# Performance work log

Measured on AMD Instinct MI355X. Metric: run time of the kernel, lower is better.

The kernel has to match this reference:

```python
import jax, jax.numpy as jnp
import numpy as np

N_NODES = 50000
N_EDGES = 400000
C = 32            # channels per irrep (scalars and l=1 vectors)
N_BASIS = 8
HID = 64          # radial MLP hidden dim
N_LAYERS = 2
N_SPECIES = 86
N_GRAPHS = 64
R_MAX = 5.0
EPS = 1e-5


def setup_inputs() -> dict:
    key = jax.random.key(0)
    ks = jax.random.split(key, 16)
    species = jax.random.randint(ks[0], (N_NODES,), 0, N_SPECIES)
    pos = jax.random.normal(ks[1], (N_NODES, 3), jnp.float32)
    edge_index = jax.random.randint(ks[2], (2, N_EDGES), 0, N_NODES)
    batch = jnp.sort(jax.random.randint(ks[3], (N_NODES,), 0, N_GRAPHS))

    emb = jax.random.normal(ks[4], (N_SPECIES, C), jnp.float32) * 0.1
    freqs = jnp.arange(1, N_BASIS + 1, dtype=jnp.float32) * jnp.pi / R_MAX  # trainable Bessel freqs
    rW1 = jax.random.normal(ks[5], (N_LAYERS, N_BASIS, HID), jnp.float32) / np.sqrt(N_BASIS)
    rb1 = jnp.zeros((N_LAYERS, HID), jnp.float32)
    rW2 = jax.random.normal(ks[6], (N_LAYERS, HID, HID), jnp.float32) / np.sqrt(HID)
    rb2 = jnp.zeros((N_LAYERS, HID), jnp.float32)
    rW3 = jax.random.normal(ks[7], (N_LAYERS, HID, 4 * C), jnp.float32) / np.sqrt(HID)
    rb3 = jnp.zeros((N_LAYERS, 4 * C), jnp.float32)
    Wss = jax.random.normal(ks[8], (N_LAYERS, C, C), jnp.float32) / np.sqrt(C)
    bss = jnp.zeros((N_LAYERS, C), jnp.float32)
    Wvv = jax.random.normal(ks[9], (N_LAYERS, C, C), jnp.float32) / np.sqrt(C)
    bn_gs = jnp.ones((N_LAYERS, C), jnp.float32)
    bn_bs = jnp.zeros((N_LAYERS, C), jnp.float32)
    bn_gv = jnp.ones((N_LAYERS, C), jnp.float32)
    W_out = jax.random.normal(ks[10], (C, 1), jnp.float32) / np.sqrt(C)
    b_out = jnp.zeros((1,), jnp.float32)
    atom_ref = jnp.zeros((N_SPECIES, 1), jnp.float32)  # AtomRef init zeros
    return dict(species=species, pos=pos, edge_index=edge_index, batch=batch,
                emb=emb, freqs=freqs, rW1=rW1, rb1=rb1, rW2=rW2, rb2=rb2,
                rW3=rW3, rb3=rb3, Wss=Wss, bss=bss, Wvv=Wvv,
                bn_gs=bn_gs, bn_bs=bn_bs, bn_gv=bn_gv,
                W_out=W_out, b_out=b_out, atom_ref=atom_ref)


def _bessel_basis(dist, freqs):
    # basis = sin(f*r)/r with smooth polynomial cutoff (as in BesselRadialBasis.forward)
    d = jnp.clip(dist, 0.0)
    basis = jnp.sin(freqs[None, :] * d[:, None]) / jnp.clip(d, 1e-6)[:, None]
    x = jnp.clip(d / R_MAX, 0.0, 1.0)
    cut = 1.0 - 6.0 * x ** 5 + 15.0 * x ** 4 - 10.0 * x ** 3
    cut = jnp.where(d <= R_MAX, cut, 0.0)
    return basis * cut[:, None]


def _forward(species, pos, edge_index, batch, emb, freqs, rW1, rb1, rW2, rb2,
             rW3, rb3, Wss, bss, Wvv, bn_gs, bn_bs, bn_gv, W_out, b_out, atom_ref):
    src, dst = edge_index[0], edge_index[1]
    vec = pos[dst] - pos[src]                      # (E,3) edge vectors
    dist = jnp.sqrt(jnp.sum(vec * vec, axis=-1))   # (E,)
    basis = _bessel_basis(dist, freqs)             # (E,NB)
    Y1 = vec / jnp.clip(dist, 1e-9)[:, None]       # (E,3) l=1 spherical harmonics (unit dir)

    s = emb[species]                               # (N,C) scalar features
    v = jnp.zeros((s.shape[0], C, 3), s.dtype)     # (N,C,3) l=1 features

    for l in range(N_LAYERS):
        # radial MLP -> per-edge channel-wise tensor-product weights (4 paths x C)
        h = jax.nn.silu(basis @ rW1[l] + rb1[l])
        h = jax.nn.silu(h @ rW2[l] + rb2[l])
        w = h @ rW3[l] + rb3[l]                    # (E,4C)
        w1, w2, w3, w4 = jnp.split(w, 4, axis=-1)  # each (E,C)

        xs = s[src]                                # (E,C)   gather
        xv = v[src]                                # (E,C,3) gather
        # TP paths: s*Y0 -> scalar; (v.Y1) -> gate scalar; s*Y1 -> vector; v*Y0 -> vector
        m_sf = w1 * xs                                               # (E,C)
        m_sg = w2 * jnp.einsum('ecd,ed->ec', xv, Y1)                 # (E,C)
        m_v = w3[..., None] * xs[..., None] * Y1[:, None, :] + w4[..., None] * xv  # (E,C,3)

        agg_sf = jax.ops.segment_sum(m_sf, dst, num_segments=N_NODES)
        agg_sg = jax.ops.segment_sum(m_sg, dst, num_segments=N_NODES)
        agg_v = jax.ops.segment_sum(m_v, dst, num_segments=N_NODES)

        # gated nonlinearity: silu on scalars, sigmoid gate on vectors
        s_new = jax.nn.silu(agg_sf)
        v_new = jax.nn.sigmoid(agg_sg)[..., None] * agg_v

        # self-interaction (equivariant linear mixing over channels)
        s_new = s_new @ Wss[l] + bss[l]
        v_new = jnp.einsum('ncd,cm->nmd', v_new, Wvv[l])

        # e3nn-style batch norm: standardize scalars; norm-normalize vectors
        mu = jnp.mean(s_new, axis=0)
        var = jnp.mean((s_new - mu) ** 2, axis=0)
        s_new = (s_new - mu) / jnp.sqrt(var + EPS) * bn_gs[l] + bn_bs[l]
        vnorm2 = jnp.mean(jnp.sum(v_new * v_new, axis=-1), axis=0) / 3.0  # per-channel, /(2l+1)
        v_new = v_new / jnp.sqrt(vnorm2 + EPS)[None, :, None] * bn_gv[l][None, :, None]

        # residual (irreps match)
        s = s + s_new
        v = v + v_new

    node_e = s @ W_out + b_out                                       # (N,1)
    graph_e = jax.ops.segment_sum(node_e, batch, num_segments=N_GRAPHS)
    ref_e = jax.ops.segment_sum(atom_ref[species], batch, num_segments=N_GRAPHS)
    return graph_e + ref_e                                           # (B,1)


def reference(species, pos, edge_index, batch, emb, freqs, rW1, rb1, rW2, rb2,
              rW3, rb3, Wss, bss, Wvv, bn_gs, bn_bs, bn_gv, W_out, b_out, atom_ref):
    return _forward(species, pos, edge_index, batch, emb, freqs, rW1, rb1, rW2, rb2,
                    rW3, rb3, Wss, bss, Wvv, bn_gs, bn_bs, bn_gv, W_out, b_out, atom_ref)
```

## Files before the change

### kernel.cpp

```cpp
#include <hip/hip_runtime.h>
#include <math.h>

#define N_NODES 50000
#define N_EDGES 400000
#define C 32
#define NB 8
#define HID 64
#define NL 2
#define NG 64
#define RMAXF 5.0f
#define EPSF 1e-5f
#define TBL 4096
#define BN_BLOCKS 512
#define NBLK_N ((N_NODES + 255) / 256)

__device__ __forceinline__ float silu_f(float x) { return x / (1.0f + __expf(-x)); }
__device__ __forceinline__ float sigmoid_f(float x) { return 1.0f / (1.0f + __expf(-x)); }
__device__ __forceinline__ void atomAddF(float* p, float val) {
  __hip_atomic_fetch_add(p, val, __ATOMIC_RELAXED, __HIP_MEMORY_SCOPE_AGENT);
}
__device__ __forceinline__ void atomAddD(double* p, double val) {
  __hip_atomic_fetch_add(p, val, __ATOMIC_RELAXED, __HIP_MEMORY_SCOPE_AGENT);
}

__global__ __launch_bounds__(256) void k_edge_geom(
    const float* __restrict__ pos, const int* __restrict__ ei,
    const float* __restrict__ freqs,
    float* __restrict__ basis, float* __restrict__ Y1, float* __restrict__ distb)
{
  int e = blockIdx.x * 256 + threadIdx.x;
  if (e >= N_EDGES) return;
  int s = ei[e], d = ei[N_EDGES + e];
  float vx = pos[d*3+0] - pos[s*3+0];
  float vy = pos[d*3+1] - pos[s*3+1];
  float vz = pos[d*3+2] - pos[s*3+2];
  float dist = sqrtf(vx*vx + vy*vy + vz*vz);
  float invd = 1.0f / fmaxf(dist, 1e-9f);
  Y1[e*3+0] = vx*invd; Y1[e*3+1] = vy*invd; Y1[e*3+2] = vz*invd;
  distb[e] = dist;
  float x = fminf(fmaxf(dist * (1.0f/RMAXF), 0.0f), 1.0f);
  float x2 = x*x, x3 = x2*x;
  float cut = 1.0f - x3 * (10.0f - 15.0f*x + 6.0f*x2);
  if (dist > RMAXF) cut = 0.0f;
  float rinv = cut / fmaxf(dist, 1e-6f);
  #pragma unroll
  for (int k = 0; k < NB; k++)
    basis[e*NB + k] = sinf(freqs[k] * dist) * rinv;
}

__global__ __launch_bounds__(256) void k_node_init(
    const int* __restrict__ species, const float* __restrict__ emb, float* __restrict__ s)
{
  int i = blockIdx.x * 256 + threadIdx.x;
  if (i >= N_NODES * C) return;
  int n = i >> 5, c = i & 31;
  s[i] = emb[species[n]*C + c];
}

__global__ __launch_bounds__(256) void k_hist(const int* __restrict__ ei, int* __restrict__ counts)
{
  int e = blockIdx.x * 256 + threadIdx.x;
  if (e >= N_EDGES) return;
  atomicAdd(&counts[ei[N_EDGES + e]], 1);
}

__global__ __launch_bounds__(256) void k_scanA(const int* __restrict__ counts, int* __restrict__ bsum)
{
  __shared__ int sh[256];
  int i = blockIdx.x * 256 + threadIdx.x;
  int x = (i < N_NODES) ? counts[i] : 0;
  sh[threadIdx.x] = x;
  __syncthreads();
  for (int off = 128; off > 0; off >>= 1) {
    if (threadIdx.x < off) sh[threadIdx.x] += sh[threadIdx.x + off];
    __syncthreads();
  }
  if (threadIdx.x == 0) bsum[blockIdx.x] = sh[0];
}

__global__ void k_scanB(int* __restrict__ bsum)
{
  if (threadIdx.x == 0) {
    int acc = 0;
    for (int b = 0; b < NBLK_N; b++) { int t = bsum[b]; bsum[b] = acc; acc += t; }
  }
}

__global__ __launch_bounds__(256) void k_scanC(const int* __restrict__ counts,
                                               const int* __restrict__ bsum,
                                               int* __restrict__ row_start)
{
  __shared__ int sh[256];
  int i = blockIdx.x * 256 + threadIdx.x;
  int x = (i < N_NODES) ? counts[i] : 0;
  sh[threadIdx.x] = x;
  __syncthreads();
  for (int off = 1; off < 256; off <<= 1) {
    int y = (threadIdx.x >= off) ? sh[threadIdx.x - off] : 0;
    __syncthreads();
    sh[threadIdx.x] += y;
    __syncthreads();
  }
  if (i < N_NODES) row_start[i] = bsum[blockIdx.x] + sh[threadIdx.x] - x;
}

__global__ __launch_bounds__(256) void k_scatter(const int* __restrict__ ei,
                                                 const int* __restrict__ row_start,
                                                 int* __restrict__ cursor,
                                                 const float* __restrict__ Y1,
                                                 const float* __restrict__ distb,
                                                 int* __restrict__ srcs,
                                                 float* __restrict__ Y1s,
                                                 float* __restrict__ dist_s)
{
  int e = blockIdx.x * 256 + threadIdx.x;
  if (e >= N_EDGES) return;
  int d = ei[N_EDGES + e];
  int p = row_start[d] + atomicAdd(&cursor[d], 1);
  srcs[p] = ei[e];
  dist_s[p] = distb[e];
  Y1s[p*3+0] = Y1[e*3+0];
  Y1s[p*3+1] = Y1[e*3+1];
  Y1s[p*3+2] = Y1[e*3+2];
}

__global__ __launch_bounds__(256) void k_table_h(
    const float* __restrict__ freqs,
    const float* __restrict__ rW1, const float* __restrict__ rb1,
    const float* __restrict__ rW2, const float* __restrict__ rb2,
    float* __restrict__ h2tab)
{
  int idx = blockIdx.x * 256 + threadIdx.x;
  if (idx >= NL * TBL) return;
  int l = idx / TBL, i = idx - l * TBL;
  float d = (float)i * (RMAXF / (float)(TBL - 1));
  float x = fminf(fmaxf(d * (1.0f/RMAXF), 0.0f), 1.0f);
  float x2 = x*x, x3 = x2*x;
  float cut = 1.0f - x3 * (10.0f - 15.0f*x + 6.0f*x2);
  float rinv = cut / fmaxf(d, 1e-6f);
  float bas[NB];
  #pragma unroll
  for (int k = 0; k < NB; k++) bas[k] = sinf(freqs[k] * d) * rinv;

  const float* W1 = rW1 + l*NB*HID;
  const float* B1 = rb1 + l*HID;
  const float* W2 = rW2 + l*HID*HID;
  const float* B2 = rb2 + l*HID;

  float h2[HID];
  #pragma unroll
  for (int j = 0; j < HID; j++) h2[j] = B2[j];
  #pragma unroll 2
  for (int k = 0; k < HID; k++) {
    float t = B1[k];
    #pragma unroll
    for (int b = 0; b < NB; b++) t = fmaf(bas[b], W1[b*HID + k], t);
    float h1k = silu_f(t);
    const float* r = W2 + k*HID;
    #pragma unroll
    for (int j = 0; j < HID; j++) h2[j] = fmaf(h1k, r[j], h2[j]);
  }
  float* out = h2tab + (size_t)idx * HID;
  #pragma unroll
  for (int j = 0; j < HID; j++) out[j] = silu_f(h2[j]);
}

__global__ __launch_bounds__(256) void k_table_w(
    const float* __restrict__ h2tab,
    const float* __restrict__ rW3, const float* __restrict__ rb3,
    float* __restrict__ wtab)
{
  int idx = blockIdx.x * 256 + threadIdx.x;
  if (idx >= NL * TBL * 16) return;
  int chunk = idx & 15;
  int row   = idx >> 4;
  int l     = row / TBL;
  const float* h2 = h2tab + (size_t)row * HID;
  const float* W3 = rW3 + l*HID*4*C + chunk*8;
  const float* B3 = rb3 + l*4*C + chunk*8;
  float a[8];
  #pragma unroll
  for (int ci = 0; ci < 8; ci++) a[ci] = B3[ci];
  #pragma unroll 4
  for (int k = 0; k < HID; k++) {
    float h = h2[k];
    #pragma unroll
    for (int ci = 0; ci < 8; ci++) a[ci] = fmaf(h, W3[k*4*C + ci], a[ci]);
  }
  float* out = wtab + (size_t)row * 128 + chunk*8;
  #pragma unroll
  for (int ci = 0; ci < 8; ci++) out[ci] = a[ci];
}

__global__ __launch_bounds__(256) void k_agg_update(
    const float* __restrict__ tb,
    const float* __restrict__ dist_s, const float* __restrict__ Y1s,
    const int* __restrict__ srcs,
    const int* __restrict__ row_start, const int* __restrict__ counts,
    const float* __restrict__ s, const float* __restrict__ v,
    const float* __restrict__ Wss, const float* __restrict__ bss,
    const float* __restrict__ Wvv,
    float* __restrict__ s_new, float* __restrict__ v_new)
{
  int t = blockIdx.x * 256 + threadIdx.x;
  int n = t >> 5;
  int c = t & 31;

  const float SCALE = (float)(TBL - 1) / RMAXF;
  float asf = 0.0f, asg = 0.0f, av0 = 0.0f, av1 = 0.0f, av2 = 0.0f;
  int beg = row_start[n], cnt = counts[n];

  int i = 0;
  for (; i + 1 < cnt; i += 2) {
    int pA = beg + i, pB = beg + i + 1;
    float dA = dist_s[pA],  dB = dist_s[pB];
    int srcA = srcs[pA],    srcB = srcs[pB];
    float yA0 = Y1s[pA*3+0], yA1 = Y1s[pA*3+1], yA2 = Y1s[pA*3+2];
    float yB0 = Y1s[pB*3+0], yB1 = Y1s[pB*3+1], yB2 = Y1s[pB*3+2];

    float tsA = fminf(dA, RMAXF) * SCALE;
    int t0A = (int)tsA; t0A = t0A > TBL-2 ? TBL-2 : t0A;
    float frA = tsA - (float)t0A;
    float tsB = fminf(dB, RMAXF) * SCALE;
    int t0B = (int)tsB; t0B = t0B > TBL-2 ? TBL-2 : t0B;
    float frB = tsB - (float)t0B;

    const float* rA0 = tb + (size_t)t0A * 128 + c;
    const float* rA1 = rA0 + 128;
    const float* rB0 = tb + (size_t)t0B * 128 + c;
    const float* rB1 = rB0 + 128;

    float a00 = rA0[0],  a01 = rA1[0];
    float a10 = rA0[32], a11 = rA1[32];
    float a20 = rA0[64], a21 = rA1[64];
    float a30 = rA0[96], a31 = rA1[96];
    float b00 = rB0[0],  b01 = rB1[0];
    float b10 = rB0[32], b11 = rB1[32];
    float b20 = rB0[64], b21 = rB1[64];
    float b30 = rB0[96], b31 = rB1[96];

    float xsA = s[srcA*C + c];
    const float* vpA = v + (size_t)(srcA*C + c)*3;
    float xvA0 = vpA[0], xvA1 = vpA[1], xvA2 = vpA[2];
    float xsB = s[srcB*C + c];
    const float* vpB = v + (size_t)(srcB*C + c)*3;
    float xvB0 = vpB[0], xvB1 = vpB[1], xvB2 = vpB[2];

    float w1A = fmaf(frA, a01-a00, a00);
    float w2A = fmaf(frA, a11-a10, a10);
    float w3A = fmaf(frA, a21-a20, a20);
    float w4A = fmaf(frA, a31-a30, a30);
    asf = fmaf(w1A, xsA, asf);
    asg = fmaf(w2A, xvA0*yA0 + xvA1*yA1 + xvA2*yA2, asg);
    float w3xsA = w3A * xsA;
    av0 += fmaf(w3xsA, yA0, w4A*xvA0);
    av1 += fmaf(w3xsA, yA1, w4A*xvA1);
    av2 += fmaf(w3xsA, yA2, w4A*xvA2);

    float w1B = fmaf(frB, b01-b00, b00);
    float w2B = fmaf(frB, b11-b10, b10);
    float w3B = fmaf(frB, b21-b20, b20);
    float w4B = fmaf(frB, b31-b30, b30);
    asf = fmaf(w1B, xsB, asf);
    asg = fmaf(w2B, xvB0*yB0 + xvB1*yB1 + xvB2*yB2, asg);
    float w3xsB = w3B * xsB;
    av0 += fmaf(w3xsB, yB0, w4B*xvB0);
    av1 += fmaf(w3xsB, yB1, w4B*xvB1);
    av2 += fmaf(w3xsB, yB2, w4B*xvB2);
  }
  if (i < cnt) {
    int p = beg + i;
    float d  = dist_s[p];
    int src = srcs[p];
    float y0 = Y1s[p*3+0], y1 = Y1s[p*3+1], y2 = Y1s[p*3+2];
    float ts = fminf(d, RMAXF) * SCALE;
    int   t0 = (int)ts; t0 = t0 > TBL-2 ? TBL-2 : t0;
    float fr = ts - (float)t0;
    const float* r0 = tb + (size_t)t0 * 128 + c;
    const float* r1 = r0 + 128;
    float w1 = fmaf(fr, r1[0]  - r0[0],  r0[0]);
    float w2 = fmaf(fr, r1[32] - r0[32], r0[32]);
    float w3 = fmaf(fr, r1[64] - r0[64], r0[64]);
    float w4 = fmaf(fr, r1[96] - r0[96], r0[96]);
    float xs = s[src*C + c];
    const float* vp = v + (size_t)(src*C + c)*3;
    float xv0 = vp[0], xv1 = vp[1], xv2 = vp[2];
    asf = fmaf(w1, xs, asf);
    asg = fmaf(w2, xv0*y0 + xv1*y1 + xv2*y2, asg);
    float w3xs = w3 * xs;
    av0 += fmaf(w3xs, y0, w4*xv0);
    av1 += fmaf(w3xs, y1, w4*xv1);
    av2 += fmaf(w3xs, y2, w4*xv2);
  }

  float sgv  = silu_f(asf);
  float gate = sigmoid_f(asg);
  float vg0 = gate*av0, vg1 = gate*av1, vg2 = gate*av2;

  float sn = bss[c];
  float vm0 = 0.0f, vm1 = 0.0f, vm2 = 0.0f;
  #pragma unroll
  for (int k = 0; k < C; k++) {
    float a  = __shfl(sgv, k, 32);
    sn = fmaf(a, Wss[k*C + c], sn);
    float wv = Wvv[k*C + c];
    vm0 = fmaf(__shfl(vg0, k, 32), wv, vm0);
    vm1 = fmaf(__shfl(vg1, k, 32), wv, vm1);
    vm2 = fmaf(__shfl(vg2, k, 32), wv, vm2);
  }

  s_new[n*C + c] = sn;
  float* vo = v_new + (size_t)(n*C + c)*3;
  vo[0] = vm0; vo[1] = vm1; vo[2] = vm2;
}

__global__ __launch_bounds__(256) void k_bn_stats(
    const float* __restrict__ s_new, const float* __restrict__ v_new,
    double* __restrict__ bn_sums)
{
  __shared__ float lacc[3*C];
  if (threadIdx.x < 3*C) lacc[threadIdx.x] = 0.0f;
  __syncthreads();
  int c = threadIdx.x & 31;
  float r1 = 0.0f, r2 = 0.0f, r3 = 0.0f;
  const int NC = N_NODES * C;
  for (int i = blockIdx.x * 256 + threadIdx.x; i < NC; i += BN_BLOCKS * 256) {
    float sn = s_new[i];
    const float* vp = v_new + (size_t)i * 3;
    r1 += sn;
    r2 += sn * sn;
    r3 += vp[0]*vp[0] + vp[1]*vp[1] + vp[2]*vp[2];
  }
  atomicAdd(&lacc[c],       r1);
  atomicAdd(&lacc[C + c],   r2);
  atomicAdd(&lacc[2*C + c], r3);
  __syncthreads();
  if (threadIdx.x < 3*C) atomAddD(&bn_sums[threadIdx.x], (double)lacc[threadIdx.x]);
}

__global__ void k_bn_scales(const double* __restrict__ bn_sums,
                            const float* __restrict__ gs, const float* __restrict__ gv,
                            float* __restrict__ scales)
{
  int m = threadIdx.x;
  if (m >= C) return;
  double S1 = bn_sums[m], S2 = bn_sums[C + m], VN = bn_sums[2*C + m];
  double mu  = S1 / (double)N_NODES;
  double var = S2 / (double)N_NODES - mu*mu;
  double vn2 = VN / (3.0 * (double)N_NODES);
  scales[m]       = (float)mu;
  scales[C + m]   = gs[m] / sqrtf((float)var + EPSF);
  scales[2*C + m] = gv[m] / sqrtf((float)vn2 + EPSF);
}

__global__ __launch_bounds__(256) void k_apply(
    const float* __restrict__ s_new, const float* __restrict__ v_new,
    const float* __restrict__ scales, const float* __restrict__ bn_bs,
    float* __restrict__ s, float* __restrict__ v)
{
  int i = blockIdx.x * 256 + threadIdx.x;
  if (i >= N_NODES * C) return;
  int c = i & 31;
  s[i] += (s_new[i] - scales[c]) * scales[C + c] + bn_bs[c];
  float vs = scales[2*C + c];
  v[(size_t)i*3+0] += v_new[(size_t)i*3+0] * vs;
  v[(size_t)i*3+1] += v_new[(size_t)i*3+1] * vs;
  v[(size_t)i*3+2] += v_new[(size_t)i*3+2] * vs;
}

__global__ __launch_bounds__(256) void k_readout(
    const float* __restrict__ s, const int* __restrict__ species,
    const int* __restrict__ batch,
    const float* __restrict__ W_out, const float* __restrict__ b_out,
    const float* __restrict__ atom_ref, float* __restrict__ out)
{
  __shared__ float acc[NG];
  if (threadIdx.x < NG) acc[threadIdx.x] = 0.0f;
  __syncthreads();
  int n = blockIdx.x * 256 + threadIdx.x;
  if (n < N_NODES) {
    float e = b_out[0] + atom_ref[species[n]];
    #pragma unroll
    for (int c = 0; c < C; c++) e = fmaf(s[n*C + c], W_out[c], e);
    atomicAdd(&acc[batch[n]], e);
  }
  __syncthreads();
  if (threadIdx.x < NG) {
    float a = acc[threadIdx.x];
    if (a != 0.0f) atomAddF(&out[threadIdx.x], a);
  }
}

__global__ __launch_bounds__(256) void k_edge_msg_fb(
    const float* __restrict__ basis, const float* __restrict__ Y1,
    const int* __restrict__ ei,
    const float* __restrict__ s, const float* __restrict__ v,
    const float* __restrict__ rW1, const float* __restrict__ rb1,
    const float* __restrict__ rW2, const float* __restrict__ rb2,
    const float* __restrict__ rW3, const float* __restrict__ rb3,
    float* __restrict__ agg_sf, float* __restrict__ agg_sg, float* __restrict__ agg_v)
{
  int e = blockIdx.x * 256 + threadIdx.x;
  if (e >= N_EDGES) return;
  int src = ei[e], dst = ei[N_EDGES + e];
  const float4 b0 = *(const float4*)(basis + (size_t)e*NB);
  const float4 b1 = *(const float4*)(basis + (size_t)e*NB + 4);
  float bas[NB] = {b0.x, b0.y, b0.z, b0.w, b1.x, b1.y, b1.z, b1.w};
  float h2[HID];
  #pragma unroll
  for (int j = 0; j < HID; j++) h2[j] = rb2[j];
  #pragma unroll 2
  for (int k = 0; k < HID; k++) {
    float t = rb1[k];
    #pragma unroll
    for (int b = 0; b < NB; b++) t = fmaf(bas[b], rW1[b*HID + k], t);
    float h1k = silu_f(t);
    const float* r = rW2 + k*HID;
    #pragma unroll
    for (int j = 0; j < HID; j++) h2[j] = fmaf(h1k, r[j], h2[j]);
  }
  #pragma unroll
  for (int j = 0; j < HID; j++) h2[j] = silu_f(h2[j]);
  float y0 = Y1[e*3+0], y1 = Y1[e*3+1], y2 = Y1[e*3+2];
  #pragma unroll 1
  for (int cb = 0; cb < 16; cb++) {
    float a[8];
    #pragma unroll
    for (int ci = 0; ci < 8; ci++) a[ci] = rb3[cb*8 + ci];
    #pragma unroll
    for (int k = 0; k < HID; k++) {
      float h = h2[k];
      #pragma unroll
      for (int ci = 0; ci < 8; ci++) a[ci] = fmaf(h, rW3[k*4*C + cb*8 + ci], a[ci]);
    }
    #pragma unroll
    for (int ci = 0; ci < 8; ci++) {
      int o = cb*8 + ci;
      int path = o >> 5;
      int c = o & 31;
      float xs = s[src*C + c];
      const float* vp = v + (size_t)(src*C + c)*3;
      float xv0 = vp[0], xv1 = vp[1], xv2 = vp[2];
      if (path == 0) {
        atomAddF(&agg_sf[dst*C + c], a[ci] * xs);
      } else if (path == 1) {
        atomAddF(&agg_sg[dst*C + c], a[ci] * (xv0*y0 + xv1*y1 + xv2*y2));
      } else if (path == 2) {
        float w3xs = a[ci] * xs;
        float* ap = agg_v + (size_t)(dst*C + c)*3;
        atomAddF(ap+0, w3xs*y0); atomAddF(ap+1, w3xs*y1); atomAddF(ap+2, w3xs*y2);
      } else {
        float* ap = agg_v + (size_t)(dst*C + c)*3;
        atomAddF(ap+0, a[ci]*xv0); atomAddF(ap+1, a[ci]*xv1); atomAddF(ap+2, a[ci]*xv2);
      }
    }
  }
}

__global__ __launch_bounds__(256) void k_node_update_fb(
    const float* __restrict__ agg_sf, const float* __restrict__ agg_sg,
    const float* __restrict__ agg_v,
    const float* __restrict__ Wss, const float* __restrict__ bss,
    const float* __restrict__ Wvv,
    float* __restrict__ s_new, float* __restrict__ v_new,
    double* __restrict__ bn_sums)
{
  __shared__ float lacc[3*C];
  int t = blockIdx.x * 256 + threadIdx.x;
  int n = t >> 5;
  int c = t & 31;
  if (threadIdx.x < 3*C) lacc[threadIdx.x] = 0.0f;
  __syncthreads();
  float asf = agg_sf[n*C + c];
  float asg = agg_sg[n*C + c];
  const float* ap = agg_v + (size_t)(n*C + c)*3;
  float av0 = ap[0], av1 = ap[1], av2 = ap[2];
  float sgv = silu_f(asf);
  float gate = sigmoid_f(asg);
  float vg0 = gate*av0, vg1 = gate*av1, vg2 = gate*av2;
  float sn = bss[c];
  float vm0 = 0.0f, vm1 = 0.0f, vm2 = 0.0f;
  #pragma unroll
  for (int k = 0; k < C; k++) {
    float a  = __shfl(sgv, k, 32);
    sn = fmaf(a, Wss[k*C + c], sn);
    float wv = Wvv[k*C + c];
    vm0 = fmaf(__shfl(vg0, k, 32), wv, vm0);
    vm1 = fmaf(__shfl(vg1, k, 32), wv, vm1);
    vm2 = fmaf(__shfl(vg2, k, 32), wv, vm2);
  }
  s_new[n*C + c] = sn;
  float* vo = v_new + (size_t)(n*C + c)*3;
  vo[0] = vm0; vo[1] = vm1; vo[2] = vm2;
  float vn2 = vm0*vm0 + vm1*vm1 + vm2*vm2;
  atomicAdd(&lacc[c], sn);
  atomicAdd(&lacc[C + c], sn*sn);
  atomicAdd(&lacc[2*C + c], vn2);
  __syncthreads();
  if (threadIdx.x < 3*C) atomAddD(&bn_sums[threadIdx.x], (double)lacc[threadIdx.x]);
}

extern "C" void kernel_launch(void* const* d_in, const int* in_sizes, int n_in,
                              void* d_out, int out_size, void* d_ws, size_t ws_size,
                              hipStream_t stream)
{
  const int*   species  = (const int*)  d_in[0];
  const float* pos      = (const float*)d_in[1];
  const int*   ei       = (const int*)  d_in[2];
  const int*   batch    = (const int*)  d_in[3];
  const float* emb      = (const float*)d_in[4];
  const float* freqs    = (const float*)d_in[5];
  const float* rW1      = (const float*)d_in[6];
  const float* rb1      = (const float*)d_in[7];
  const float* rW2      = (const float*)d_in[8];
  const float* rb2      = (const float*)d_in[9];
  const float* rW3      = (const float*)d_in[10];
  const float* rb3      = (const float*)d_in[11];
  const float* Wss      = (const float*)d_in[12];
  const float* bss      = (const float*)d_in[13];
  const float* Wvv      = (const float*)d_in[14];
  const float* bn_gs    = (const float*)d_in[15];
  const float* bn_bs    = (const float*)d_in[16];
  const float* bn_gv    = (const float*)d_in[17];
  const float* W_out    = (const float*)d_in[18];
  const float* b_out    = (const float*)d_in[19];
  const float* atom_ref = (const float*)d_in[20];

  float* ws = (float*)d_ws;
  size_t off = 0;
  float* basis  = ws + off; off += (size_t)N_EDGES * NB;
  float* Y1     = ws + off; off += (size_t)N_EDGES * 3;
  float* distb  = ws + off; off += (size_t)N_EDGES;
  float* s      = ws + off; off += (size_t)N_NODES * C;
  float* v      = ws + off; off += (size_t)N_NODES * C * 3;
  float* s_new  = ws + off; off += (size_t)N_NODES * C;
  float* v_new  = ws + off; off += (size_t)N_NODES * C * 3;
  double* bn_sums = (double*)(ws + off); off += 192;
  float* scales = ws + off; off += 96;

  size_t ra = off;
  float* Y1s      = ws + ra;            ra += (size_t)N_EDGES * 3;
  float* dist_s   = ws + ra;            ra += (size_t)N_EDGES;
  int*   srcs     = (int*)(ws + ra);    ra += N_EDGES;
  int*   counts   = (int*)(ws + ra);    ra += N_NODES;
  int*   row_start= (int*)(ws + ra);    ra += N_NODES;
  int*   cursor   = (int*)(ws + ra);    ra += N_NODES;
  int*   bsum     = (int*)(ws + ra);    ra += 256;
  float* h2tab    = ws + ra;            ra += (size_t)NL * TBL * HID;
  float* wtab     = ws + ra;            ra += (size_t)NL * TBL * 128;
  size_t req_sorted = ra * 4;

  size_t rb = off;
  float* agg_sf = ws + rb; rb += (size_t)N_NODES * C;
  float* agg_sg = ws + rb; rb += (size_t)N_NODES * C;
  float* agg_v  = ws + rb; rb += (size_t)N_NODES * C * 3;

  dim3 b256(256);
  const int gE  = (N_EDGES + 255) / 256;
  const int gNC = (N_NODES * C + 255) / 256;
  const int gN  = (N_NODES + 255) / 256;

  hipMemsetAsync(v, 0, (size_t)N_NODES * C * 3 * sizeof(float), stream);
  k_edge_geom<<<gE, b256, 0, stream>>>(pos, ei, freqs, basis, Y1, distb);
  k_node_init<<<gNC, b256, 0, stream>>>(species, emb, s);

  if (ws_size >= req_sorted) {
    hipMemsetAsync(counts, 0, N_NODES * sizeof(int), stream);
    hipMemsetAsync(cursor, 0, N_NODES * sizeof(int), stream);
    k_hist<<<gE, b256, 0, stream>>>(ei, counts);
    k_scanA<<<NBLK_N, b256, 0, stream>>>(counts, bsum);
    k_scanB<<<1, 64, 0, stream>>>(bsum);
    k_scanC<<<NBLK_N, b256, 0, stream>>>(counts, bsum, row_start);
    k_scatter<<<gE, b256, 0, stream>>>(ei, row_start, cursor, Y1, distb,
                                       srcs, Y1s, dist_s);
    k_table_h<<<(NL*TBL)/256, b256, 0, stream>>>(freqs, rW1, rb1, rW2, rb2, h2tab);
    k_table_w<<<(NL*TBL*16)/256, b256, 0, stream>>>(h2tab, rW3, rb3, wtab);

    for (int l = 0; l < NL; l++) {
      hipMemsetAsync(bn_sums, 0, 96 * sizeof(double), stream);
      k_agg_update<<<(N_NODES*C)/256, b256, 0, stream>>>(
          wtab + (size_t)l * TBL * 128, dist_s, Y1s, srcs,
          row_start, counts, s, v, Wss + l*C*C, bss + l*C, Wvv + l*C*C,
          s_new, v_new);
      k_bn_stats<<<BN_BLOCKS, b256, 0, stream>>>(s_new, v_new, bn_sums);
      k_bn_scales<<<1, 64, 0, stream>>>(bn_sums, bn_gs + l*C, bn_gv + l*C, scales);
      k_apply<<<gNC, b256, 0, stream>>>(s_new, v_new, scales, bn_bs + l*C, s, v);
    }
  } else {
    for (int l = 0; l < NL; l++) {
      hipMemsetAsync(agg_sf, 0, (size_t)N_NODES * 5 * C * sizeof(float), stream);
      hipMemsetAsync(bn_sums, 0, 96 * sizeof(double), stream);
      k_edge_msg_fb<<<gE, b256, 0, stream>>>(basis, Y1, ei, s, v,
          rW1 + l*NB*HID, rb1 + l*HID, rW2 + l*HID*HID, rb2 + l*HID,
          rW3 + l*HID*4*C, rb3 + l*4*C, agg_sf, agg_sg, agg_v);
      k_node_update_fb<<<(N_NODES*C)/256, b256, 0, stream>>>(agg_sf, agg_sg, agg_v,
          Wss + l*C*C, bss + l*C, Wvv + l*C*C, s_new, v_new, bn_sums);
      k_bn_scales<<<1, 64, 0, stream>>>(bn_sums, bn_gs + l*C, bn_gv + l*C, scales);
      k_apply<<<gNC, b256, 0, stream>>>(s_new, v_new, scales, bn_bs + l*C, s, v);
    }
  }

  hipMemsetAsync(d_out, 0, NG * sizeof(float), stream);
  k_readout<<<gN, b256, 0, stream>>>(s, species, batch, W_out, b_out, atom_ref, (float*)d_out);
}
```

Baseline: 337.7 us.

## Gather node features in bf16, fuse geometry into scatter, fold BN scales into apply

Keeps bf16 shadow copies of s and v, written by node_init and apply, so the edge aggregation gathers half as many bytes per source node. Edge geometry is now computed inside the scatter kernel, which drops the separate geometry pass and the intermediate Y1/dist buffers on the sorted path. The single-block BN-scales kernel is folded into apply, and the single-thread serial block-sum scan becomes a parallel 256-thread scan. The bf16 gathers reduce precision of the messages, and apply now writes an extra bf16 copy.

```diff
diff --git a/kernel.cpp b/kernel.cpp
--- a/kernel.cpp
+++ b/kernel.cpp
@@ -22,11 +22,18 @@
 __device__ __forceinline__ void atomAddD(double* p, double val) {
   __hip_atomic_fetch_add(p, val, __ATOMIC_RELAXED, __HIP_MEMORY_SCOPE_AGENT);
 }
+__device__ __forceinline__ unsigned short bf16_rne(float f) {
+  unsigned u = __float_as_uint(f);
+  return (unsigned short)((u + 0x7FFFu + ((u >> 16) & 1u)) >> 16);
+}
+__device__ __forceinline__ float bfu(unsigned short u) {
+  return __uint_as_float(((unsigned)u) << 16);
+}
 
 __global__ __launch_bounds__(256) void k_edge_geom(
     const float* __restrict__ pos, const int* __restrict__ ei,
     const float* __restrict__ freqs,
-    float* __restrict__ basis, float* __restrict__ Y1, float* __restrict__ distb)
+    float* __restrict__ basis, float* __restrict__ Y1)
 {
   int e = blockIdx.x * 256 + threadIdx.x;
   if (e >= N_EDGES) return;
@@ -37,7 +44,6 @@
   float dist = sqrtf(vx*vx + vy*vy + vz*vz);
   float invd = 1.0f / fmaxf(dist, 1e-9f);
   Y1[e*3+0] = vx*invd; Y1[e*3+1] = vy*invd; Y1[e*3+2] = vz*invd;
-  distb[e] = dist;
   float x = fminf(fmaxf(dist * (1.0f/RMAXF), 0.0f), 1.0f);
   float x2 = x*x, x3 = x2*x;
   float cut = 1.0f - x3 * (10.0f - 15.0f*x + 6.0f*x2);
@@ -49,12 +55,15 @@
 }
 
 __global__ __launch_bounds__(256) void k_node_init(
-    const int* __restrict__ species, const float* __restrict__ emb, float* __restrict__ s)
+    const int* __restrict__ species, const float* __restrict__ emb,
+    float* __restrict__ s, unsigned short* __restrict__ s_bf)
 {
   int i = blockIdx.x * 256 + threadIdx.x;
   if (i >= N_NODES * C) return;
   int n = i >> 5, c = i & 31;
-  s[i] = emb[species[n]*C + c];
+  float x = emb[species[n]*C + c];
+  s[i] = x;
+  s_bf[i] = bf16_rne(x);
 }
 
 __global__ __launch_bounds__(256) void k_hist(const int* __restrict__ ei, int* __restrict__ counts)
@@ -78,12 +87,20 @@
   if (threadIdx.x == 0) bsum[blockIdx.x] = sh[0];
 }
 
-__global__ void k_scanB(int* __restrict__ bsum)
-{
-  if (threadIdx.x == 0) {
-    int acc = 0;
-    for (int b = 0; b < NBLK_N; b++) { int t = bsum[b]; bsum[b] = acc; acc += t; }
-  }
+__global__ __launch_bounds__(256) void k_scanB(int* __restrict__ bsum)
+{
+  __shared__ int sh[256];
+  int tid = threadIdx.x;
+  int x = (tid < NBLK_N) ? bsum[tid] : 0;
+  sh[tid] = x;
+  __syncthreads();
+  for (int off = 1; off < 256; off <<= 1) {
+    int y = (tid >= off) ? sh[tid - off] : 0;
+    __syncthreads();
+    sh[tid] += y;
+    __syncthreads();
+  }
+  if (tid < NBLK_N) bsum[tid] = sh[tid] - x;
 }
 
 __global__ __launch_bounds__(256) void k_scanC(const int* __restrict__ counts,
@@ -104,24 +121,25 @@
   if (i < N_NODES) row_start[i] = bsum[blockIdx.x] + sh[threadIdx.x] - x;
 }
 
-__global__ __launch_bounds__(256) void k_scatter(const int* __restrict__ ei,
-                                                 const int* __restrict__ row_start,
-                                                 int* __restrict__ cursor,
-                                                 const float* __restrict__ Y1,
-                                                 const float* __restrict__ distb,
-                                                 int* __restrict__ srcs,
-                                                 float* __restrict__ Y1s,
-                                                 float* __restrict__ dist_s)
+__global__ __launch_bounds__(256) void k_geom_scatter(
+    const float* __restrict__ pos, const int* __restrict__ ei,
+    const int* __restrict__ row_start, int* __restrict__ cursor,
+    int* __restrict__ srcs, float* __restrict__ Y1s, float* __restrict__ dist_s)
 {
   int e = blockIdx.x * 256 + threadIdx.x;
   if (e >= N_EDGES) return;
-  int d = ei[N_EDGES + e];
+  int s = ei[e], d = ei[N_EDGES + e];
+  float vx = pos[d*3+0] - pos[s*3+0];
+  float vy = pos[d*3+1] - pos[s*3+1];
+  float vz = pos[d*3+2] - pos[s*3+2];
+  float dist = sqrtf(vx*vx + vy*vy + vz*vz);
+  float invd = 1.0f / fmaxf(dist, 1e-9f);
   int p = row_start[d] + atomicAdd(&cursor[d], 1);
-  srcs[p] = ei[e];
-  dist_s[p] = distb[e];
-  Y1s[p*3+0] = Y1[e*3+0];
-  Y1s[p*3+1] = Y1[e*3+1];
-  Y1s[p*3+2] = Y1[e*3+2];
+  srcs[p] = s;
+  dist_s[p] = dist;
+  Y1s[p*3+0] = vx*invd;
+  Y1s[p*3+1] = vy*invd;
+  Y1s[p*3+2] = vz*invd;
 }
 
 __global__ __launch_bounds__(256) void k_table_h(
@@ -197,7 +215,7 @@
     const float* __restrict__ dist_s, const float* __restrict__ Y1s,
     const int* __restrict__ srcs,
     const int* __restrict__ row_start, const int* __restrict__ counts,
-    const float* __restrict__ s, const float* __restrict__ v,
+    const unsigned short* __restrict__ s_bf, const unsigned short* __restrict__ v_bf,
     const float* __restrict__ Wss, const float* __restrict__ bss,
     const float* __restrict__ Wvv,
     float* __restrict__ s_new, float* __restrict__ v_new)
@@ -239,12 +257,12 @@
     float b20 = rB0[64], b21 = rB1[64];
     float b30 = rB0[96], b31 = rB1[96];
 
-    float xsA = s[srcA*C + c];
-    const float* vpA = v + (size_t)(srcA*C + c)*3;
-    float xvA0 = vpA[0], xvA1 = vpA[1], xvA2 = vpA[2];
-    float xsB = s[srcB*C + c];
-    const float* vpB = v + (size_t)(srcB*C + c)*3;
-    float xvB0 = vpB[0], xvB1 = vpB[1], xvB2 = vpB[2];
+    float xsA = bfu(s_bf[srcA*C + c]);
+    const unsigned short* vpA = v_bf + (size_t)(srcA*C + c)*3;
+    float xvA0 = bfu(vpA[0]), xvA1 = bfu(vpA[1]), xvA2 = bfu(vpA[2]);
+    float xsB = bfu(s_bf[srcB*C + c]);
+    const unsigned short* vpB = v_bf + (size_t)(srcB*C + c)*3;
+    float xvB0 = bfu(vpB[0]), xvB1 = bfu(vpB[1]), xvB2 = bfu(vpB[2]);
 
     float w1A = fmaf(frA, a01-a00, a00);
     float w2A = fmaf(frA, a11-a10, a10);
@@ -282,9 +300,9 @@
     float w2 = fmaf(fr, r1[32] - r0[32], r0[32]);
     float w3 = fmaf(fr, r1[64] - r0[64], r0[64]);
     float w4 = fmaf(fr, r1[96] - r0[96], r0[96]);
-    float xs = s[src*C + c];
-    const float* vp = v + (size_t)(src*C + c)*3;
-    float xv0 = vp[0], xv1 = vp[1], xv2 = vp[2];
+    float xs = bfu(s_bf[src*C + c]);
+    const unsigned short* vp = v_bf + (size_t)(src*C + c)*3;
+    float xv0 = bfu(vp[0]), xv1 = bfu(vp[1]), xv2 = bfu(vp[2]);
     asf = fmaf(w1, xs, asf);
     asg = fmaf(w2, xv0*y0 + xv1*y1 + xv2*y2, asg);
     float w3xs = w3 * xs;
@@ -338,34 +356,36 @@
   if (threadIdx.x < 3*C) atomAddD(&bn_sums[threadIdx.x], (double)lacc[threadIdx.x]);
 }
 
-__global__ void k_bn_scales(const double* __restrict__ bn_sums,
-                            const float* __restrict__ gs, const float* __restrict__ gv,
-                            float* __restrict__ scales)
-{
-  int m = threadIdx.x;
-  if (m >= C) return;
-  double S1 = bn_sums[m], S2 = bn_sums[C + m], VN = bn_sums[2*C + m];
-  double mu  = S1 / (double)N_NODES;
-  double var = S2 / (double)N_NODES - mu*mu;
-  double vn2 = VN / (3.0 * (double)N_NODES);
-  scales[m]       = (float)mu;
-  scales[C + m]   = gs[m] / sqrtf((float)var + EPSF);
-  scales[2*C + m] = gv[m] / sqrtf((float)vn2 + EPSF);
-}
-
 __global__ __launch_bounds__(256) void k_apply(
     const float* __restrict__ s_new, const float* __restrict__ v_new,
-    const float* __restrict__ scales, const float* __restrict__ bn_bs,
-    float* __restrict__ s, float* __restrict__ v)
+    const double* __restrict__ bn_sums,
+    const float* __restrict__ gs, const float* __restrict__ gv,
+    const float* __restrict__ bn_bs,
+    float* __restrict__ s, float* __restrict__ v,
+    unsigned short* __restrict__ s_bf, unsigned short* __restrict__ v_bf)
 {
   int i = blockIdx.x * 256 + threadIdx.x;
   if (i >= N_NODES * C) return;
   int c = i & 31;
-  s[i] += (s_new[i] - scales[c]) * scales[C + c] + bn_bs[c];
-  float vs = scales[2*C + c];
-  v[(size_t)i*3+0] += v_new[(size_t)i*3+0] * vs;
-  v[(size_t)i*3+1] += v_new[(size_t)i*3+1] * vs;
-  v[(size_t)i*3+2] += v_new[(size_t)i*3+2] * vs;
+  double S1 = bn_sums[c], S2 = bn_sums[C + c], VN = bn_sums[2*C + c];
+  float mu  = (float)(S1 / (double)N_NODES);
+  float var = (float)(S2 / (double)N_NODES) - mu*mu;
+  float vn2 = (float)(VN / (3.0 * (double)N_NODES));
+  float ssc = gs[c] / sqrtf(var + EPSF);
+  float vsc = gv[c] / sqrtf(vn2 + EPSF);
+
+  float sv = s[i] + (s_new[i] - mu) * ssc + bn_bs[c];
+  s[i] = sv;
+  s_bf[i] = bf16_rne(sv);
+  float* vp = v + (size_t)i*3;
+  const float* vn = v_new + (size_t)i*3;
+  unsigned short* vb = v_bf + (size_t)i*3;
+  #pragma unroll
+  for (int d = 0; d < 3; d++) {
+    float vv = vp[d] + vn[d] * vsc;
+    vp[d] = vv;
+    vb[d] = bf16_rne(vv);
+  }
 }
 
 __global__ __launch_bounds__(256) void k_readout(
@@ -498,6 +518,36 @@
   atomicAdd(&lacc[2*C + c], vn2);
   __syncthreads();
   if (threadIdx.x < 3*C) atomAddD(&bn_sums[threadIdx.x], (double)lacc[threadIdx.x]);
+}
+
+__global__ void k_bn_scales_fb(const double* __restrict__ bn_sums,
+                               const float* __restrict__ gs, const float* __restrict__ gv,
+                               float* __restrict__ scales)
+{
+  int m = threadIdx.x;
+  if (m >= C) return;
+  double S1 = bn_sums[m], S2 = bn_sums[C + m], VN = bn_sums[2*C + m];
+  double mu  = S1 / (double)N_NODES;
+  double var = S2 / (double)N_NODES - mu*mu;
+  double vn2 = VN / (3.0 * (double)N_NODES);
+  scales[m]       = (float)mu;
+  scales[C + m]   = gs[m] / sqrtf((float)var + EPSF);
+  scales[2*C + m] = gv[m] / sqrtf((float)vn2 + EPSF);
+}
+
+__global__ __launch_bounds__(256) void k_apply_fb(
+    const float* __restrict__ s_new, const float* __restrict__ v_new,
+    const float* __restrict__ scales, const float* __restrict__ bn_bs,
+    float* __restrict__ s, float* __restrict__ v)
+{
+  int i = blockIdx.x * 256 + threadIdx.x;
+  if (i >= N_NODES * C) return;
+  int c = i & 31;
+  s[i] += (s_new[i] - scales[c]) * scales[C + c] + bn_bs[c];
+  float vs = scales[2*C + c];
+  v[(size_t)i*3+0] += v_new[(size_t)i*3+0] * vs;
+  v[(size_t)i*3+1] += v_new[(size_t)i*3+1] * vs;
+  v[(size_t)i*3+2] += v_new[(size_t)i*3+2] * vs;
 }
 
 extern "C" void kernel_launch(void* const* d_in, const int* in_sizes, int n_in,
@@ -530,7 +580,6 @@
   size_t off = 0;
   float* basis  = ws + off; off += (size_t)N_EDGES * NB;
   float* Y1     = ws + off; off += (size_t)N_EDGES * 3;
-  float* distb  = ws + off; off += (size_t)N_EDGES;
   float* s      = ws + off; off += (size_t)N_NODES * C;
   float* v      = ws + off; off += (size_t)N_NODES * C * 3;
   float* s_new  = ws + off; off += (size_t)N_NODES * C;
@@ -548,6 +597,8 @@
   int*   bsum     = (int*)(ws + ra);    ra += 256;
   float* h2tab    = ws + ra;            ra += (size_t)NL * TBL * HID;
   float* wtab     = ws + ra;            ra += (size_t)NL * TBL * 128;
+  unsigned short* s_bf = (unsigned short*)(ws + ra); ra += (size_t)N_NODES * C / 2;
+  unsigned short* v_bf = (unsigned short*)(ws + ra); ra += (size_t)N_NODES * C * 3 / 2;
   size_t req_sorted = ra * 4;
 
   size_t rb = off;
@@ -561,18 +612,18 @@
   const int gN  = (N_NODES + 255) / 256;
 
   hipMemsetAsync(v, 0, (size_t)N_NODES * C * 3 * sizeof(float), stream);
-  k_edge_geom<<<gE, b256, 0, stream>>>(pos, ei, freqs, basis, Y1, distb);
-  k_node_init<<<gNC, b256, 0, stream>>>(species, emb, s);
 
   if (ws_size >= req_sorted) {
+    hipMemsetAsync(v_bf, 0, (size_t)N_NODES * C * 3 * sizeof(unsigned short), stream);
     hipMemsetAsync(counts, 0, N_NODES * sizeof(int), stream);
     hipMemsetAsync(cursor, 0, N_NODES * sizeof(int), stream);
+    k_node_init<<<gNC, b256, 0, stream>>>(species, emb, s, s_bf);
     k_hist<<<gE, b256, 0, stream>>>(ei, counts);
     k_scanA<<<NBLK_N, b256, 0, stream>>>(counts, bsum);
-    k_scanB<<<1, 64, 0, stream>>>(bsum);
+    k_scanB<<<1, b256, 0, stream>>>(bsum);
     k_scanC<<<NBLK_N, b256, 0, stream>>>(counts, bsum, row_start);
-    k_scatter<<<gE, b256, 0, stream>>>(ei, row_start, cursor, Y1, distb,
-                                       srcs, Y1s, dist_s);
+    k_geom_scatter<<<gE, b256, 0, stream>>>(pos, ei, row_start, cursor,
+                                            srcs, Y1s, dist_s);
     k_table_h<<<(NL*TBL)/256, b256, 0, stream>>>(freqs, rW1, rb1, rW2, rb2, h2tab);
     k_table_w<<<(NL*TBL*16)/256, b256, 0, stream>>>(h2tab, rW3, rb3, wtab);
 
@@ -580,13 +631,15 @@
       hipMemsetAsync(bn_sums, 0, 96 * sizeof(double), stream);
       k_agg_update<<<(N_NODES*C)/256, b256, 0, stream>>>(
           wtab + (size_t)l * TBL * 128, dist_s, Y1s, srcs,
-          row_start, counts, s, v, Wss + l*C*C, bss + l*C, Wvv + l*C*C,
+          row_start, counts, s_bf, v_bf, Wss + l*C*C, bss + l*C, Wvv + l*C*C,
           s_new, v_new);
       k_bn_stats<<<BN_BLOCKS, b256, 0, stream>>>(s_new, v_new, bn_sums);
-      k_bn_scales<<<1, 64, 0, stream>>>(bn_sums, bn_gs + l*C, bn_gv + l*C, scales);
-      k_apply<<<gNC, b256, 0, stream>>>(s_new, v_new, scales, bn_bs + l*C, s, v);
+      k_apply<<<gNC, b256, 0, stream>>>(s_new, v_new, bn_sums,
+          bn_gs + l*C, bn_gv + l*C, bn_bs + l*C, s, v, s_bf, v_bf);
     }
   } else {
+    k_node_init<<<gNC, b256, 0, stream>>>(species, emb, s, (unsigned short*)(ws + off));
+    k_edge_geom<<<gE, b256, 0, stream>>>(pos, ei, freqs, basis, Y1);
     for (int l = 0; l < NL; l++) {
       hipMemsetAsync(agg_sf, 0, (size_t)N_NODES * 5 * C * sizeof(float), stream);
       hipMemsetAsync(bn_sums, 0, 96 * sizeof(double), stream);
@@ -595,8 +648,8 @@
           rW3 + l*HID*4*C, rb3 + l*4*C, agg_sf, agg_sg, agg_v);
       k_node_update_fb<<<(N_NODES*C)/256, b256, 0, stream>>>(agg_sf, agg_sg, agg_v,
           Wss + l*C*C, bss + l*C, Wvv + l*C*C, s_new, v_new, bn_sums);
-      k_bn_scales<<<1, 64, 0, stream>>>(bn_sums, bn_gs + l*C, bn_gv + l*C, scales);
-      k_apply<<<gNC, b256, 0, stream>>>(s_new, v_new, scales, bn_bs + l*C, s, v);
+      k_bn_scales_fb<<<1, 64, 0, stream>>>(bn_sums, bn_gs + l*C, bn_gv + l*C, scales);
+      k_apply_fb<<<gNC, b256, 0, stream>>>(s_new, v_new, scales, bn_bs + l*C, s, v);
     }
   }
 
```

Result: no change. 332.5 us (-1.5%).
